# Kernel optimization log

Hardware: AMD Instinct MI355X
Metric: run time of the kernel (lower is better)

## Reference

```python
import jax, jax.numpy as jnp
import numpy as np

N_USERS = 100000
N_ITEMS = 50000
N_NODES = N_USERS + N_ITEMS
D = 32
N_EDGES = 8000000
N_LAYERS = 3
B = 65536


def setup_inputs() -> dict:
    key = jax.random.key(0)
    ks = jax.random.split(key, 9)
    users = jax.random.randint(ks[0], (B,), 0, N_USERS)
    items = jax.random.randint(ks[1], (B,), 0, N_ITEMS)
    # COO sparse normalized adjacency (symmetric bipartite graph in LightGCN)
    rows = jax.random.randint(ks[2], (N_EDGES,), 0, N_NODES)
    cols = jax.random.randint(ks[3], (N_EDGES,), 0, N_NODES)
    # normalized values ~ 1/sqrt(deg_i*deg_j); keep small so propagation is stable
    vals = jax.random.uniform(ks[4], (N_EDGES,), dtype=jnp.float32) * 0.01
    # embedding tables, init std=0.1 per nn.init.normal_(std=0.1)
    user_emb = jax.random.normal(ks[5], (N_USERS, D), dtype=jnp.float32) * 0.1
    item_emb = jax.random.normal(ks[6], (N_ITEMS, D), dtype=jnp.float32) * 0.1
    # per-user denormalization stats (norm_mode='users')
    norm_means = jax.random.normal(ks[7], (N_USERS,), dtype=jnp.float32)
    norm_stds = jax.random.uniform(ks[8], (N_USERS,), dtype=jnp.float32) + 0.5
    return {
        "users": users, "items": items,
        "rows": rows, "cols": cols, "vals": vals,
        "user_emb": user_emb, "item_emb": item_emb,
        "norm_means": norm_means, "norm_stds": norm_stds,
    }


def _spmm(rows, cols, vals, x):
    # sparse COO matmul: out[i] = sum_{e: rows[e]==i} vals[e] * x[cols[e]]
    return jax.ops.segment_sum(vals[:, None] * x[cols], rows, num_segments=N_NODES)


def reference(users, items, rows, cols, vals, user_emb, item_emb, norm_means, norm_stds):
    all_emb = jnp.concatenate([user_emb, item_emb], axis=0)  # [N, D]
    acc = all_emb
    emb_sum = all_emb
    for _ in range(N_LAYERS):
        acc = _spmm(rows, cols, vals, acc)
        emb_sum = emb_sum + acc
    light_out = emb_sum / jnp.asarray(N_LAYERS + 1, dtype=all_emb.dtype)
    all_users = light_out[:N_USERS]
    all_items = light_out[N_USERS:]
    gamma = jnp.sum(all_users[users] * all_items[items], axis=1)  # [B]
    # norm_mode == 'users' -> index stats by users
    return gamma * norm_stds[users] + norm_means[users]
```

## Files before the change

kernel.cpp:

```cpp
#include <hip/hip_runtime.h>
#include <hip/hip_fp16.h>

#define N_USERS 100000
#define N_ITEMS 50000
#define N_NODES 150000
#define DIM 32
#define N_EDGES 8000000
#define B_OUT 65536

#define NB 1024
#define RPB 147
#define CH 8192
#define N_PBLK ((N_EDGES + CH - 1) / CH)
#define PART_T 1024
#define EPT (CH / PART_T)
#define MS_T 1024
#define T 256
#define NRED 8
#define RS_LD (NB + 1)
#define NPANEL 3
#define NBIN (RPB * NPANEL)
#define BUFE 8448
#define VQ_SCALE 1638400.0f
#define VQ_INV   6.103515625e-7f
#define WSCALE1 (VQ_INV * 8.0f)
#define WSCALE2 (VQ_INV * 32.0f)
#define WSCALE3 (VQ_INV * 32.0f)
#define INV1 (1.0f / 64.0f)
#define INV2 (1.0f / 2048.0f)
#define INV3 (1.0f / 65536.0f)

__device__ __forceinline__ unsigned enc_h(unsigned u16) {
    return (u16 + 0x7Fu + ((u16 >> 8) & 1u)) >> 8;
}
__device__ __forceinline__ unsigned enc_f(float x) {
    return enc_h((unsigned)__half_as_ushort(__float2half(x)));
}
__device__ __forceinline__ float dec_b(unsigned b) {
    return __half2float(__ushort_as_half((unsigned short)(b << 8)));
}
__device__ __forceinline__ int panel_of(int col) {
    return (col >= 100000) ? 2 : ((col >= 50000) ? 1 : 0);
}

__global__ void init_kernel(const float* __restrict__ user_emb,
                            const float* __restrict__ item_emb,
                            unsigned char* __restrict__ x_a) {
    int i = blockIdx.x * blockDim.x + threadIdx.x;
    const int total = N_NODES * DIM / 8;
    if (i >= total) return;
    const int user8 = N_USERS * DIM / 8;
    const float4* src = (i < user8) ? ((const float4*)user_emb + (size_t)i * 2)
                                    : ((const float4*)item_emb + (size_t)(i - user8) * 2);
    float4 a = src[0], b = src[1];
    unsigned w0 = enc_f(a.x * 8.f) | (enc_f(a.y * 8.f) << 8)
                | (enc_f(a.z * 8.f) << 16) | (enc_f(a.w * 8.f) << 24);
    unsigned w1 = enc_f(b.x * 8.f) | (enc_f(b.y * 8.f) << 8)
                | (enc_f(b.z * 8.f) << 16) | (enc_f(b.w * 8.f) << 24);
    uint2 o; o.x = w0; o.y = w1;
    ((uint2*)x_a)[i] = o;
}

__global__ void __launch_bounds__(PART_T)
part_kernel(const int* __restrict__ rows,
            const int* __restrict__ cols,
            const float* __restrict__ vals,
            int* __restrict__ runstart,
            int2* __restrict__ bucket_ev) {
    __shared__ int2 buf[CH];
    __shared__ int hist[NB];
    __shared__ int wsum[16];
    const int tid   = threadIdx.x;
    const int chunk = blockIdx.x;
    const int e0    = chunk * CH;
    const int ecnt  = (N_EDGES - e0 < CH) ? (N_EDGES - e0) : CH;
    const int lane  = tid & 63, wid = tid >> 6;

    hist[tid] = 0;
    __syncthreads();

    int myrow[EPT];
    #pragma unroll
    for (int j = 0; j < EPT; ++j) {
        int idx = j * PART_T + tid;
        int r = (idx < ecnt) ? rows[e0 + idx] : -1;
        myrow[j] = r;
        if (r >= 0) atomicAdd(&hist[(unsigned)r / RPB], 1);
    }
    __syncthreads();

    int v = hist[tid];
    int inc = v;
    #pragma unroll
    for (int off = 1; off < 64; off <<= 1) {
        int t = __shfl_up(inc, off, 64);
        if (lane >= off) inc += t;
    }
    if (lane == 63) wsum[wid] = inc;
    __syncthreads();
    if (wid == 0) {
        int s = (lane < 16) ? wsum[lane] : 0;
        #pragma unroll
        for (int off = 1; off < 16; off <<= 1) {
            int t = __shfl_up(s, off, 64);
            if (lane >= off) s += t;
        }
        if (lane < 16) wsum[lane] = s;
    }
    __syncthreads();
    int base = (wid > 0) ? wsum[wid - 1] : 0;
    int incl = base + inc;
    int excl = incl - v;
    runstart[(size_t)chunk * RS_LD + tid] = e0 + excl;
    if (tid == NB - 1) runstart[(size_t)chunk * RS_LD + NB] = e0 + incl;
    hist[tid] = excl;
    __syncthreads();

    #pragma unroll
    for (int j = 0; j < EPT; ++j) {
        int r = myrow[j];
        if (r < 0) continue;
        int idx = j * PART_T + tid;
        unsigned b = (unsigned)r / RPB;
        int k = atomicAdd(&hist[b], 1);
        int2 ev;
        ev.x = (int)(((unsigned)(r - (int)b * RPB) << 18) | (unsigned)cols[e0 + idx]);
        ev.y = __float_as_int(vals[e0 + idx]);
        buf[k] = ev;
    }
    __syncthreads();

    const int n4 = ecnt >> 1;
    const int4* b4 = (const int4*)buf;
    int4* g4 = (int4*)(bucket_ev + e0);
    for (int i = tid; i < n4; i += PART_T) g4[i] = b4[i];
}

__global__ void btot_kernel(const int* __restrict__ runstart, int* __restrict__ partial) {
    const int b = threadIdx.x;
    const int g = blockIdx.x;
    int c = 0;
    for (int ch = g; ch < N_PBLK; ch += NRED)
        c += runstart[(size_t)ch * RS_LD + b + 1] - runstart[(size_t)ch * RS_LD + b];
    partial[g * NB + b] = c;
}

__global__ void bscan_kernel(const int* __restrict__ partial,
                             int* __restrict__ bcsr,
                             int* __restrict__ row_ptr) {
    __shared__ int wsum[16];
    const int tid = threadIdx.x;
    const int lane = tid & 63, wid = tid >> 6;
    int v = 0;
    #pragma unroll
    for (int g = 0; g < NRED; ++g) v += partial[g * NB + tid];
    int inc = v;
    #pragma unroll
    for (int off = 1; off < 64; off <<= 1) {
        int t = __shfl_up(inc, off, 64);
        if (lane >= off) inc += t;
    }
    if (lane == 63) wsum[wid] = inc;
    __syncthreads();
    if (wid == 0) {
        int s = (lane < 16) ? wsum[lane] : 0;
        #pragma unroll
        for (int off = 1; off < 16; off <<= 1) {
            int t = __shfl_up(s, off, 64);
            if (lane >= off) s += t;
        }
        if (lane < 16) wsum[lane] = s;
    }
    __syncthreads();
    int base = (wid > 0) ? wsum[wid - 1] : 0;
    bcsr[tid] = base + inc - v;
    if (tid == 0) row_ptr[N_NODES] = N_EDGES;
}

__global__ void __launch_bounds__(MS_T)
mini_scatter_kernel(const int* __restrict__ runstart,
                    const int2* __restrict__ bucket_ev,
                    const int* __restrict__ bcsr,
                    int* __restrict__ row_ptr,
                    unsigned* __restrict__ csr_w) {
    __shared__ int2 ibuf[BUFE];
    __shared__ unsigned sbuf[BUFE];
    __shared__ int rs0[N_PBLK];
    __shared__ int ofs[N_PBLK];
    __shared__ int rlen[N_PBLK];
    __shared__ int cnt2[NBIN];
    __shared__ int cur2[NBIN];
    __shared__ int wsum[MS_T / 64];
    const int b   = blockIdx.x;
    const int tid = threadIdx.x;
    const int lane = tid & 63, wid = tid >> 6;

    for (int i = tid; i < N_PBLK; i += MS_T) {
        int a = runstart[(size_t)i * RS_LD + b];
        rs0[i]  = a;
        rlen[i] = runstart[(size_t)i * RS_LD + b + 1] - a;
    }
    if (tid < NBIN) cnt2[tid] = 0;
    __syncthreads();

    int lv = (tid < N_PBLK) ? rlen[tid] : 0;
    int linc = lv;
    #pragma unroll
    for (int off = 1; off < 64; off <<= 1) {
        int t = __shfl_up(linc, off, 64);
        if (lane >= off) linc += t;
    }
    if (lane == 63) wsum[wid] = linc;
    __syncthreads();
    if (wid == 0) {
        int s = (lane < MS_T / 64) ? wsum[lane] : 0;
        #pragma unroll
        for (int off = 1; off < MS_T / 64; off <<= 1) {
            int t = __shfl_up(s, off, 64);
            if (lane >= off) s += t;
        }
        if (lane < MS_T / 64) wsum[lane] = s;
    }
    __syncthreads();
    int lbase = (wid > 0) ? wsum[wid - 1] : 0;
    if (tid < N_PBLK) ofs[tid] = lbase + linc - lv;
    __syncthreads();
    const int cnt = ofs[N_PBLK - 1] + rlen[N_PBLK - 1];
    __syncthreads();

    const int grp8 = tid >> 3, ln8 = tid & 7;
    const int cb = bcsr[b];

    if (cnt <= BUFE) {
        for (int c = grp8; c < N_PBLK; c += (MS_T / 8)) {
            int s0 = rs0[c], o0 = ofs[c], L = rlen[c];
            for (int i = ln8; i < L; i += 8) ibuf[o0 + i] = bucket_ev[s0 + i];
        }
        __syncthreads();
        for (int i = tid; i < cnt; i += MS_T) {
            unsigned key = (unsigned)ibuf[i].x;
            atomicAdd(&cnt2[((int)(key >> 18)) * NPANEL + panel_of((int)(key & 0x3FFFFu))], 1);
        }
    } else {
        for (int c = grp8; c < N_PBLK; c += (MS_T / 8)) {
            int s0 = rs0[c], L = rlen[c];
            for (int i = ln8; i < L; i += 8) {
                unsigned key = (unsigned)bucket_ev[s0 + i].x;
                atomicAdd(&cnt2[((int)(key >> 18)) * NPANEL + panel_of((int)(key & 0x3FFFFu))], 1);
            }
        }
    }
    __syncthreads();

    int v = (tid < NBIN) ? cnt2[tid] : 0;
    int inc = v;
    #pragma unroll
    for (int off = 1; off < 64; off <<= 1) {
        int t = __shfl_up(inc, off, 64);
        if (lane >= off) inc += t;
    }
    if (lane == 63) wsum[wid] = inc;
    __syncthreads();
    if (wid == 0) {
        int s = (lane < MS_T / 64) ? wsum[lane] : 0;
        #pragma unroll
        for (int off = 1; off < MS_T / 64; off <<= 1) {
            int t = __shfl_up(s, off, 64);
            if (lane >= off) s += t;
        }
        if (lane < MS_T / 64) wsum[lane] = s;
    }
    __syncthreads();
    int base = (wid > 0) ? wsum[wid - 1] : 0;
    if (tid < NBIN) {
        int excl = base + inc - v;
        cur2[tid] = excl;
        if (tid % NPANEL == 0) {
            int r = b * RPB + tid / NPANEL;
            if (r < N_NODES) row_ptr[r] = cb + excl;
        }
    }
    __syncthreads();

    if (cnt <= BUFE) {
        for (int i = tid; i < cnt; i += MS_T) {
            int2 ev = ibuf[i];
            unsigned key = (unsigned)ev.x;
            int rl  = (int)(key >> 18);
            int col = (int)(key & 0x3FFFFu);
            float vv = __int_as_float(ev.y);
            int q = (int)(vv * VQ_SCALE + 0.5f);
            if (q > 16383) q = 16383;
            int pos = atomicAdd(&cur2[rl * NPANEL + panel_of(col)], 1);
            sbuf[pos] = ((unsigned)col << 14) | (unsigned)q;
        }
        __syncthreads();
        unsigned* g = csr_w + cb;
        for (int i = tid; i < cnt; i += MS_T) g[i] = sbuf[i];
    } else {
        for (int c = grp8; c < N_PBLK; c += (MS_T / 8)) {
            int s0 = rs0[c], L = rlen[c];
            for (int i = ln8; i < L; i += 8) {
                int2 ev = bucket_ev[s0 + i];
                unsigned key = (unsigned)ev.x;
                int rl  = (int)(key >> 18);
                int col = (int)(key & 0x3FFFFu);
                float vv = __int_as_float(ev.y);
                int q = (int)(vv * VQ_SCALE + 0.5f);
                if (q > 16383) q = 16383;
                int pos = atomicAdd(&cur2[rl * NPANEL + panel_of(col)], 1);
                csr_w[cb + pos] = ((unsigned)col << 14) | (unsigned)q;
            }
        }
    }
}

__global__ void spmm_kernel(const int* __restrict__ row_ptr,
                            const unsigned* __restrict__ csr,
                            const unsigned char* __restrict__ xin,
                            unsigned char* __restrict__ xout,
                            float wscale) {
    int tid = blockIdx.x * blockDim.x + threadIdx.x;
    int row = tid >> 5;
    if (row >= N_NODES) return;
    const int ll  = tid & 31;
    const int j   = ll >> 2;
    const int seg = ll & 3;
    const int s = row_ptr[row];
    const int e = row_ptr[row + 1];
    const unsigned char* xseg = xin + seg * 8;

    __half2 acc0 = __float2half2_rn(0.f);
    __half2 acc1 = acc0, acc2 = acc0, acc3 = acc0;

    for (int i = s; i < e; i += 32) {
        int e0 = i + j, e1 = i + 8 + j, e2 = i + 16 + j, e3 = i + 24 + j;
        unsigned p0 = (e0 < e) ? csr[e0] : 0u;
        unsigned p1 = (e1 < e) ? csr[e1] : 0u;
        unsigned p2 = (e2 < e) ? csr[e2] : 0u;
        unsigned p3 = (e3 < e) ? csr[e3] : 0u;
        uint2 v0 = *(const uint2*)(xseg + ((size_t)((p0 >> 9) & ~31u)));
        uint2 v1 = *(const uint2*)(xseg + ((size_t)((p1 >> 9) & ~31u)));
        uint2 v2 = *(const uint2*)(xseg + ((size_t)((p2 >> 9) & ~31u)));
        uint2 v3 = *(const uint2*)(xseg + ((size_t)((p3 >> 9) & ~31u)));
        __half2 w0 = __float2half2_rn((float)(p0 & 0x3FFFu) * wscale);
        __half2 w1 = __float2half2_rn((float)(p1 & 0x3FFFu) * wscale);
        __half2 w2 = __float2half2_rn((float)(p2 & 0x3FFFu) * wscale);
        __half2 w3 = __float2half2_rn((float)(p3 & 0x3FFFu) * wscale);
        unsigned h;
        h = __builtin_amdgcn_perm(v0.x, v0.x, 0x010C000Cu);
        acc0 = __hfma2(w0, *(__half2*)&h, acc0);
        h = __builtin_amdgcn_perm(v0.x, v0.x, 0x030C020Cu);
        acc1 = __hfma2(w0, *(__half2*)&h, acc1);
        h = __builtin_amdgcn_perm(v0.y, v0.y, 0x010C000Cu);
        acc2 = __hfma2(w0, *(__half2*)&h, acc2);
        h = __builtin_amdgcn_perm(v0.y, v0.y, 0x030C020Cu);
        acc3 = __hfma2(w0, *(__half2*)&h, acc3);
        h = __builtin_amdgcn_perm(v1.x, v1.x, 0x010C000Cu);
        acc0 = __hfma2(w1, *(__half2*)&h, acc0);
        h = __builtin_amdgcn_perm(v1.x, v1.x, 0x030C020Cu);
        acc1 = __hfma2(w1, *(__half2*)&h, acc1);
        h = __builtin_amdgcn_perm(v1.y, v1.y, 0x010C000Cu);
        acc2 = __hfma2(w1, *(__half2*)&h, acc2);
        h = __builtin_amdgcn_perm(v1.y, v1.y, 0x030C020Cu);
        acc3 = __hfma2(w1, *(__half2*)&h, acc3);
        h = __builtin_amdgcn_perm(v2.x, v2.x, 0x010C000Cu);
        acc0 = __hfma2(w2, *(__half2*)&h, acc0);
        h = __builtin_amdgcn_perm(v2.x, v2.x, 0x030C020Cu);
        acc1 = __hfma2(w2, *(__half2*)&h, acc1);
        h = __builtin_amdgcn_perm(v2.y, v2.y, 0x010C000Cu);
        acc2 = __hfma2(w2, *(__half2*)&h, acc2);
        h = __builtin_amdgcn_perm(v2.y, v2.y, 0x030C020Cu);
        acc3 = __hfma2(w2, *(__half2*)&h, acc3);
        h = __builtin_amdgcn_perm(v3.x, v3.x, 0x010C000Cu);
        acc0 = __hfma2(w3, *(__half2*)&h, acc0);
        h = __builtin_amdgcn_perm(v3.x, v3.x, 0x030C020Cu);
        acc1 = __hfma2(w3, *(__half2*)&h, acc1);
        h = __builtin_amdgcn_perm(v3.y, v3.y, 0x010C000Cu);
        acc2 = __hfma2(w3, *(__half2*)&h, acc2);
        h = __builtin_amdgcn_perm(v3.y, v3.y, 0x030C020Cu);
        acc3 = __hfma2(w3, *(__half2*)&h, acc3);
    }

    #pragma unroll
    for (int m = 4; m <= 16; m <<= 1) {
        unsigned t;
        t = (unsigned)__shfl_xor(*(int*)&acc0, m, 64); acc0 = __hadd2(acc0, *(__half2*)&t);
        t = (unsigned)__shfl_xor(*(int*)&acc1, m, 64); acc1 = __hadd2(acc1, *(__half2*)&t);
        t = (unsigned)__shfl_xor(*(int*)&acc2, m, 64); acc2 = __hadd2(acc2, *(__half2*)&t);
        t = (unsigned)__shfl_xor(*(int*)&acc3, m, 64); acc3 = __hadd2(acc3, *(__half2*)&t);
    }

    if (j == 0) {
        unsigned a0 = *(unsigned*)&acc0, a1 = *(unsigned*)&acc1;
        unsigned a2 = *(unsigned*)&acc2, a3 = *(unsigned*)&acc3;
        unsigned w0 = enc_h(a0 & 0xFFFFu) | (enc_h(a0 >> 16) << 8)
                    | (enc_h(a1 & 0xFFFFu) << 16) | (enc_h(a1 >> 16) << 24);
        unsigned w1 = enc_h(a2 & 0xFFFFu) | (enc_h(a2 >> 16) << 8)
                    | (enc_h(a3 & 0xFFFFu) << 16) | (enc_h(a3 >> 16) << 24);
        uint2 o; o.x = w0; o.y = w1;
        *(uint2*)(xout + (size_t)row * 32 + seg * 8) = o;
    }
}

__device__ __forceinline__ void add_row8(float* s, const unsigned char* x,
                                         size_t node, float inv) {
    const uint4* p = (const uint4*)(x + node * 32);
    uint4 t0 = p[0], t1 = p[1];
    unsigned w[8] = {t0.x, t0.y, t0.z, t0.w, t1.x, t1.y, t1.z, t1.w};
    #pragma unroll
    for (int k = 0; k < 8; ++k) {
        unsigned ww = w[k];
        s[k * 4 + 0] += dec_b(ww & 0xFFu) * inv;
        s[k * 4 + 1] += dec_b((ww >> 8) & 0xFFu) * inv;
        s[k * 4 + 2] += dec_b((ww >> 16) & 0xFFu) * inv;
        s[k * 4 + 3] += dec_b(ww >> 24) * inv;
    }
}

__global__ void final_kernel(const int* __restrict__ users,
                             const int* __restrict__ items,
                             const float* __restrict__ user_emb,
                             const float* __restrict__ item_emb,
                             const unsigned char* __restrict__ x1,
                             const unsigned char* __restrict__ x2,
                             const unsigned char* __restrict__ x3,
                             const float* __restrict__ means,
                             const float* __restrict__ stds,
                             float* __restrict__ out) {
    int b = blockIdx.x * blockDim.x + threadIdx.x;
    if (b >= B_OUT) return;
    int u  = users[b];
    int itm = items[b];
    size_t un = (size_t)u;
    size_t in = (size_t)(N_USERS + itm);

    float su[DIM], si[DIM];
    const float4* eu = (const float4*)(user_emb + un * DIM);
    const float4* ei = (const float4*)(item_emb + (size_t)itm * DIM);
    #pragma unroll
    for (int k = 0; k < 8; ++k) {
        float4 a = eu[k];
        su[k * 4 + 0] = a.x; su[k * 4 + 1] = a.y; su[k * 4 + 2] = a.z; su[k * 4 + 3] = a.w;
        float4 c = ei[k];
        si[k * 4 + 0] = c.x; si[k * 4 + 1] = c.y; si[k * 4 + 2] = c.z; si[k * 4 + 3] = c.w;
    }
    add_row8(su, x1, un, INV1); add_row8(su, x2, un, INV2); add_row8(su, x3, un, INV3);
    add_row8(si, x1, in, INV1); add_row8(si, x2, in, INV2); add_row8(si, x3, in, INV3);

    float gamma = 0.f;
    #pragma unroll
    for (int d = 0; d < DIM; ++d) gamma += su[d] * si[d];
    gamma *= 0.0625f;
    out[b] = gamma * stds[u] + means[u];
}

extern "C" void kernel_launch(void* const* d_in, const int* in_sizes, int n_in,
                              void* d_out, int out_size, void* d_ws, size_t ws_size,
                              hipStream_t stream) {
    const int*   users    = (const int*)d_in[0];
    const int*   items    = (const int*)d_in[1];
    const int*   rows     = (const int*)d_in[2];
    const int*   cols     = (const int*)d_in[3];
    const float* vals     = (const float*)d_in[4];
    const float* user_emb = (const float*)d_in[5];
    const float* item_emb = (const float*)d_in[6];
    const float* means    = (const float*)d_in[7];
    const float* stds     = (const float*)d_in[8];
    float* out = (float*)d_out;

    char* w = (char*)d_ws;
    size_t off = 0;
    auto alloc = [&](size_t bytes) -> void* {
        void* p = w + off;
        off = (off + bytes + 255) & ~(size_t)255;
        return p;
    };
    size_t regionA = ((size_t)N_PBLK * CH * sizeof(int2) + 255) & ~(size_t)255;
    char* a0 = (char*)alloc(regionA);
    int2* bucket_ev = (int2*)a0;
    size_t aoff = 0;
    auto allocA = [&](size_t bytes) -> void* {
        void* p = a0 + aoff;
        aoff = (aoff + bytes + 255) & ~(size_t)255;
        return p;
    };
    unsigned char* x_a = (unsigned char*)allocA((size_t)N_NODES * DIM);
    unsigned char* x_b = (unsigned char*)allocA((size_t)N_NODES * DIM);
    unsigned char* x_c = (unsigned char*)allocA((size_t)N_NODES * DIM);
    unsigned char* x_d = (unsigned char*)allocA((size_t)N_NODES * DIM);

    int*      runstart = (int*)     alloc((size_t)N_PBLK * RS_LD * sizeof(int));
    int*      partial  = (int*)     alloc((size_t)NRED * NB * sizeof(int));
    int*      row_ptr  = (int*)     alloc((size_t)(N_NODES + 1) * sizeof(int));
    int*      bcsr     = (int*)     alloc((size_t)NB * sizeof(int));
    unsigned* csr_w    = (unsigned*)alloc((size_t)N_EDGES * sizeof(unsigned));
    (void)ws_size;

    const int g_init  = (N_NODES * DIM / 8 + T - 1) / T;
    const int g_spmm  = (N_NODES * DIM + T - 1) / T;
    const int g_final = (B_OUT + T - 1) / T;

    part_kernel<<<N_PBLK, PART_T, 0, stream>>>(rows, cols, vals, runstart, bucket_ev);
    btot_kernel<<<NRED, NB, 0, stream>>>(runstart, partial);
    bscan_kernel<<<1, NB, 0, stream>>>(partial, bcsr, row_ptr);
    mini_scatter_kernel<<<NB, MS_T, 0, stream>>>(runstart, bucket_ev, bcsr, row_ptr, csr_w);

    init_kernel<<<g_init, T, 0, stream>>>(user_emb, item_emb, x_a);
    spmm_kernel<<<g_spmm, T, 0, stream>>>(row_ptr, csr_w, x_a, x_b, WSCALE1);
    spmm_kernel<<<g_spmm, T, 0, stream>>>(row_ptr, csr_w, x_b, x_c, WSCALE2);
    spmm_kernel<<<g_spmm, T, 0, stream>>>(row_ptr, csr_w, x_c, x_d, WSCALE3);

    final_kernel<<<g_final, T, 0, stream>>>(users, items, user_emb, item_emb,
                                            x_b, x_c, x_d, means, stds, out);
}
```

Measured before the change: 283.9 us.

## Split bucket records into key and quantized value arrays, transpose run-start table

```diff
diff --git a/kernel.cpp b/kernel.cpp
--- a/kernel.cpp
+++ b/kernel.cpp
@@ -17,7 +17,6 @@
 #define MS_T 1024
 #define T 256
 #define NRED 8
-#define RS_LD (NB + 1)
 #define NPANEL 3
 #define NBIN (RPB * NPANEL)
 #define BUFE 8448
@@ -41,6 +40,10 @@
 }
 __device__ __forceinline__ int panel_of(int col) {
     return (col >= 100000) ? 2 : ((col >= 50000) ? 1 : 0);
+}
+__device__ __forceinline__ int chend(int c) {
+    int e = (c + 1) * CH;
+    return (e > N_EDGES) ? N_EDGES : e;
 }
 
 __global__ void init_kernel(const float* __restrict__ user_emb,
@@ -65,9 +68,11 @@
 part_kernel(const int* __restrict__ rows,
             const int* __restrict__ cols,
             const float* __restrict__ vals,
-            int* __restrict__ runstart,
-            int2* __restrict__ bucket_ev) {
-    __shared__ int2 buf[CH];
+            int* __restrict__ rsA,
+            unsigned* __restrict__ bucket_key,
+            unsigned short* __restrict__ bucket_q) {
+    __shared__ unsigned kbuf[CH];
+    __shared__ unsigned short qbuf[CH];
     __shared__ int hist[NB];
     __shared__ int wsum[16];
     const int tid   = threadIdx.x;
@@ -109,10 +114,8 @@
     }
     __syncthreads();
     int base = (wid > 0) ? wsum[wid - 1] : 0;
-    int incl = base + inc;
-    int excl = incl - v;
-    runstart[(size_t)chunk * RS_LD + tid] = e0 + excl;
-    if (tid == NB - 1) runstart[(size_t)chunk * RS_LD + NB] = e0 + incl;
+    int excl = base + inc - v;
+    rsA[(size_t)chunk * NB + tid] = e0 + excl;
     hist[tid] = excl;
     __syncthreads();
 
@@ -123,25 +126,45 @@
         int idx = j * PART_T + tid;
         unsigned b = (unsigned)r / RPB;
         int k = atomicAdd(&hist[b], 1);
-        int2 ev;
-        ev.x = (int)(((unsigned)(r - (int)b * RPB) << 18) | (unsigned)cols[e0 + idx]);
-        ev.y = __float_as_int(vals[e0 + idx]);
-        buf[k] = ev;
-    }
-    __syncthreads();
-
-    const int n4 = ecnt >> 1;
-    const int4* b4 = (const int4*)buf;
-    int4* g4 = (int4*)(bucket_ev + e0);
-    for (int i = tid; i < n4; i += PART_T) g4[i] = b4[i];
-}
-
-__global__ void btot_kernel(const int* __restrict__ runstart, int* __restrict__ partial) {
+        kbuf[k] = ((unsigned)(r - (int)b * RPB) << 18) | (unsigned)cols[e0 + idx];
+        float vv = vals[e0 + idx];
+        int q = (int)(vv * VQ_SCALE + 0.5f);
+        if (q > 16383) q = 16383;
+        qbuf[k] = (unsigned short)q;
+    }
+    __syncthreads();
+
+    const int4* k4 = (const int4*)kbuf;
+    int4* gk = (int4*)(bucket_key + e0);
+    for (int i = tid; i < ecnt / 4; i += PART_T) gk[i] = k4[i];
+    const int4* q4 = (const int4*)qbuf;
+    int4* gq = (int4*)(bucket_q + e0);
+    for (int i = tid; i < ecnt / 8; i += PART_T) gq[i] = q4[i];
+}
+
+__global__ void transpose_kernel(const int* __restrict__ in, int* __restrict__ out) {
+    __shared__ int t[32][33];
+    const int c0 = blockIdx.x * 32, b0 = blockIdx.y * 32;
+    for (int dy = threadIdx.y; dy < 32; dy += 8) {
+        int c = c0 + dy, b = b0 + threadIdx.x;
+        t[dy][threadIdx.x] = (c < N_PBLK) ? in[(size_t)c * NB + b] : 0;
+    }
+    __syncthreads();
+    for (int dy = threadIdx.y; dy < 32; dy += 8) {
+        int b = b0 + dy, c = c0 + threadIdx.x;
+        if (c < N_PBLK) out[(size_t)b * N_PBLK + c] = t[threadIdx.x][dy];
+    }
+}
+
+__global__ void btot_kernel(const int* __restrict__ rsA, int* __restrict__ partial) {
     const int b = threadIdx.x;
     const int g = blockIdx.x;
     int c = 0;
-    for (int ch = g; ch < N_PBLK; ch += NRED)
-        c += runstart[(size_t)ch * RS_LD + b + 1] - runstart[(size_t)ch * RS_LD + b];
+    for (int ch = g; ch < N_PBLK; ch += NRED) {
+        int s0 = rsA[(size_t)ch * NB + b];
+        int s1 = (b < NB - 1) ? rsA[(size_t)ch * NB + b + 1] : chend(ch);
+        c += s1 - s0;
+    }
     partial[g * NB + b] = c;
 }
 
@@ -178,12 +201,14 @@
 }
 
 __global__ void __launch_bounds__(MS_T)
-mini_scatter_kernel(const int* __restrict__ runstart,
-                    const int2* __restrict__ bucket_ev,
+mini_scatter_kernel(const int* __restrict__ rsT,
+                    const unsigned* __restrict__ bucket_key,
+                    const unsigned short* __restrict__ bucket_q,
                     const int* __restrict__ bcsr,
                     int* __restrict__ row_ptr,
                     unsigned* __restrict__ csr_w) {
-    __shared__ int2 ibuf[BUFE];
+    __shared__ unsigned kbuf[BUFE];
+    __shared__ unsigned short qb[BUFE];
     __shared__ unsigned sbuf[BUFE];
     __shared__ int rs0[N_PBLK];
     __shared__ int ofs[N_PBLK];
@@ -196,9 +221,11 @@
     const int lane = tid & 63, wid = tid >> 6;
 
     for (int i = tid; i < N_PBLK; i += MS_T) {
-        int a = runstart[(size_t)i * RS_LD + b];
+        int a = rsT[(size_t)b * N_PBLK + i];
+        int e = (b < NB - 1) ? rsT[(size_t)(b + 1) * N_PBLK + i]
+                             : chend(i);
         rs0[i]  = a;
-        rlen[i] = runstart[(size_t)i * RS_LD + b + 1] - a;
+        rlen[i] = e - a;
     }
     if (tid < NBIN) cnt2[tid] = 0;
     __syncthreads();
@@ -234,18 +261,21 @@
     if (cnt <= BUFE) {
         for (int c = grp8; c < N_PBLK; c += (MS_T / 8)) {
             int s0 = rs0[c], o0 = ofs[c], L = rlen[c];
-            for (int i = ln8; i < L; i += 8) ibuf[o0 + i] = bucket_ev[s0 + i];
+            for (int i = ln8; i < L; i += 8) {
+                kbuf[o0 + i] = bucket_key[s0 + i];
+                qb[o0 + i]   = bucket_q[s0 + i];
+            }
         }
         __syncthreads();
         for (int i = tid; i < cnt; i += MS_T) {
-            unsigned key = (unsigned)ibuf[i].x;
+            unsigned key = kbuf[i];
             atomicAdd(&cnt2[((int)(key >> 18)) * NPANEL + panel_of((int)(key & 0x3FFFFu))], 1);
         }
     } else {
         for (int c = grp8; c < N_PBLK; c += (MS_T / 8)) {
             int s0 = rs0[c], L = rlen[c];
             for (int i = ln8; i < L; i += 8) {
-                unsigned key = (unsigned)bucket_ev[s0 + i].x;
+                unsigned key = bucket_key[s0 + i];
                 atomicAdd(&cnt2[((int)(key >> 18)) * NPANEL + panel_of((int)(key & 0x3FFFFu))], 1);
             }
         }
@@ -284,15 +314,11 @@
 
     if (cnt <= BUFE) {
         for (int i = tid; i < cnt; i += MS_T) {
-            int2 ev = ibuf[i];
-            unsigned key = (unsigned)ev.x;
+            unsigned key = kbuf[i];
             int rl  = (int)(key >> 18);
             int col = (int)(key & 0x3FFFFu);
-            float vv = __int_as_float(ev.y);
-            int q = (int)(vv * VQ_SCALE + 0.5f);
-            if (q > 16383) q = 16383;
             int pos = atomicAdd(&cur2[rl * NPANEL + panel_of(col)], 1);
-            sbuf[pos] = ((unsigned)col << 14) | (unsigned)q;
+            sbuf[pos] = ((unsigned)col << 14) | (unsigned)qb[i];
         }
         __syncthreads();
         unsigned* g = csr_w + cb;
@@ -301,15 +327,11 @@
         for (int c = grp8; c < N_PBLK; c += (MS_T / 8)) {
             int s0 = rs0[c], L = rlen[c];
             for (int i = ln8; i < L; i += 8) {
-                int2 ev = bucket_ev[s0 + i];
-                unsigned key = (unsigned)ev.x;
+                unsigned key = bucket_key[s0 + i];
                 int rl  = (int)(key >> 18);
                 int col = (int)(key & 0x3FFFFu);
-                float vv = __int_as_float(ev.y);
-                int q = (int)(vv * VQ_SCALE + 0.5f);
-                if (q > 16383) q = 16383;
                 int pos = atomicAdd(&cur2[rl * NPANEL + panel_of(col)], 1);
-                csr_w[cb + pos] = ((unsigned)col << 14) | (unsigned)q;
+                csr_w[cb + pos] = ((unsigned)col << 14) | (unsigned)bucket_q[s0 + i];
             }
         }
     }
@@ -476,9 +498,12 @@
         off = (off + bytes + 255) & ~(size_t)255;
         return p;
     };
-    size_t regionA = ((size_t)N_PBLK * CH * sizeof(int2) + 255) & ~(size_t)255;
+    size_t keyBytes = (size_t)N_PBLK * CH * sizeof(unsigned);
+    size_t qBytes   = (size_t)N_PBLK * CH * sizeof(unsigned short);
+    size_t regionA  = ((keyBytes + 255) & ~(size_t)255) + ((qBytes + 255) & ~(size_t)255);
     char* a0 = (char*)alloc(regionA);
-    int2* bucket_ev = (int2*)a0;
+    unsigned*       bucket_key = (unsigned*)a0;
+    unsigned short* bucket_q   = (unsigned short*)(a0 + ((keyBytes + 255) & ~(size_t)255));
     size_t aoff = 0;
     auto allocA = [&](size_t bytes) -> void* {
         void* p = a0 + aoff;
@@ -490,21 +515,24 @@
     unsigned char* x_c = (unsigned char*)allocA((size_t)N_NODES * DIM);
     unsigned char* x_d = (unsigned char*)allocA((size_t)N_NODES * DIM);
 
-    int*      runstart = (int*)     alloc((size_t)N_PBLK * RS_LD * sizeof(int));
-    int*      partial  = (int*)     alloc((size_t)NRED * NB * sizeof(int));
-    int*      row_ptr  = (int*)     alloc((size_t)(N_NODES + 1) * sizeof(int));
-    int*      bcsr     = (int*)     alloc((size_t)NB * sizeof(int));
-    unsigned* csr_w    = (unsigned*)alloc((size_t)N_EDGES * sizeof(unsigned));
+    int*      rsA     = (int*)     alloc((size_t)N_PBLK * NB * sizeof(int));
+    int*      rsT     = (int*)     alloc((size_t)NB * N_PBLK * sizeof(int));
+    int*      partial = (int*)     alloc((size_t)NRED * NB * sizeof(int));
+    int*      row_ptr = (int*)     alloc((size_t)(N_NODES + 1) * sizeof(int));
+    int*      bcsr    = (int*)     alloc((size_t)NB * sizeof(int));
+    unsigned* csr_w   = (unsigned*)alloc((size_t)N_EDGES * sizeof(unsigned));
     (void)ws_size;
 
     const int g_init  = (N_NODES * DIM / 8 + T - 1) / T;
     const int g_spmm  = (N_NODES * DIM + T - 1) / T;
     const int g_final = (B_OUT + T - 1) / T;
 
-    part_kernel<<<N_PBLK, PART_T, 0, stream>>>(rows, cols, vals, runstart, bucket_ev);
-    btot_kernel<<<NRED, NB, 0, stream>>>(runstart, partial);
+    part_kernel<<<N_PBLK, PART_T, 0, stream>>>(rows, cols, vals, rsA, bucket_key, bucket_q);
+    dim3 tgrid((N_PBLK + 31) / 32, NB / 32);
+    transpose_kernel<<<tgrid, dim3(32, 8), 0, stream>>>(rsA, rsT);
+    btot_kernel<<<NRED, NB, 0, stream>>>(rsA, partial);
     bscan_kernel<<<1, NB, 0, stream>>>(partial, bcsr, row_ptr);
-    mini_scatter_kernel<<<NB, MS_T, 0, stream>>>(runstart, bucket_ev, bcsr, row_ptr, csr_w);
+    mini_scatter_kernel<<<NB, MS_T, 0, stream>>>(rsT, bucket_key, bucket_q, bcsr, row_ptr, csr_w);
 
     init_kernel<<<g_init, T, 0, stream>>>(user_emb, item_emb, x_a);
     spmm_kernel<<<g_spmm, T, 0, stream>>>(row_ptr, csr_w, x_a, x_b, WSCALE1);
```

Measured after the change: 306.9 us. +8.1%, slower.
